# Optimization experiments

Hardware: AMD Instinct MI355X
Metric: run time of the kernel (lower is better)

## Reference

```python
import jax, jax.numpy as jnp
import numpy as np

D_MODEL = 1024
HEADS = 16
D_K = D_MODEL // HEADS
B, S = 2, 2048


def setup_inputs() -> dict:
    key = jax.random.key(0)
    ks = jax.random.split(key, 11)
    sc = 1.0 / np.sqrt(D_MODEL)
    inp = {
        "q": jax.random.normal(ks[0], (B, S, D_MODEL), jnp.float32),
        "k": jax.random.normal(ks[1], (B, S, D_MODEL), jnp.float32),
        "v": jax.random.normal(ks[2], (B, S, D_MODEL), jnp.float32),
        # causal mask, broadcastable to (B, H, S, S); 0 -> masked
        "mask": jnp.tril(jnp.ones((S, S), jnp.int32))[None, None],
        "w_q": jax.random.normal(ks[3], (D_MODEL, D_MODEL), jnp.float32) * sc,
        "b_q": jax.random.normal(ks[4], (D_MODEL,), jnp.float32) * sc,
        "w_k": jax.random.normal(ks[5], (D_MODEL, D_MODEL), jnp.float32) * sc,
        "b_k": jax.random.normal(ks[6], (D_MODEL,), jnp.float32) * sc,
        "w_v": jax.random.normal(ks[7], (D_MODEL, D_MODEL), jnp.float32) * sc,
        "b_v": jax.random.normal(ks[8], (D_MODEL,), jnp.float32) * sc,
        "w_o": jax.random.normal(ks[9], (D_MODEL, D_MODEL), jnp.float32) * sc,
        "b_o": jax.random.normal(ks[10], (D_MODEL,), jnp.float32) * sc,
    }
    return inp


def reference(q, k, v, mask, w_q, b_q, w_k, b_k, w_v, b_v, w_o, b_o):
    b = q.shape[0]
    # torch Linear: x @ W.T + b
    Q = q @ w_q.T + b_q
    K = k @ w_k.T + b_k
    V = v @ w_v.T + b_v
    # (B, S, D) -> (B, H, S, d_k)
    Q = Q.reshape(b, -1, HEADS, D_K).transpose(0, 2, 1, 3)
    K = K.reshape(b, -1, HEADS, D_K).transpose(0, 2, 1, 3)
    V = V.reshape(b, -1, HEADS, D_K).transpose(0, 2, 1, 3)
    scores = jnp.einsum("bhqd,bhkd->bhqk", Q, K) / np.sqrt(D_K).astype(np.float32)
    scores = jnp.where(mask == 0, -jnp.inf, scores)
    attn = jax.nn.softmax(scores, axis=-1)
    out = jnp.einsum("bhqk,bhkd->bhqd", attn, V)
    out = out.transpose(0, 2, 1, 3).reshape(b, -1, D_MODEL)
    # dropout is identity in eval mode
    return out @ w_o.T + b_o
```

## Files before the change

kernel.cpp:

```cpp
#include <hip/hip_runtime.h>
#include <math.h>

#define D_MODEL 1024
#define N_HEADS 16
#define DKH     64
#define BATCH   2
#define SEQ     2048
#define NT      (SEQ/64)

typedef unsigned short u16;
typedef __attribute__((ext_vector_type(8))) short short8;
typedef __attribute__((ext_vector_type(4))) float f32x4;

__device__ __forceinline__ u16 f2bf(float f) {
    unsigned u = __float_as_uint(f);
    u += 0x7fffu + ((u >> 16) & 1u);
    return (u16)(u >> 16);
}

__device__ __forceinline__ void gll16(const void* g, void* l) {
    __builtin_amdgcn_global_load_lds((const __attribute__((address_space(1))) void*)g,
                                     (__attribute__((address_space(3))) void*)l, 16, 0, 0);
}

__global__ __launch_bounds__(256)
void convert_kernel(const float* __restrict__ q, const float* __restrict__ k,
                    const float* __restrict__ v, const float* __restrict__ wq,
                    const float* __restrict__ wk, const float* __restrict__ wv,
                    const float* __restrict__ wo,
                    u16* __restrict__ qb, u16* __restrict__ kb, u16* __restrict__ vb,
                    u16* __restrict__ wqb, u16* __restrict__ wkb,
                    u16* __restrict__ wvb, u16* __restrict__ wob)
{
    const size_t NV = ((size_t)16 << 20) >> 3;
    for (size_t i = (size_t)blockIdx.x * blockDim.x + threadIdx.x; i < NV;
         i += (size_t)gridDim.x * blockDim.x) {
        const size_t e = i << 3;
        const float* s; u16* d; size_t off;
        if (e < ((size_t)12 << 20)) {
            const int seg = (int)(e >> 22);
            off = e & (((size_t)1 << 22) - 1);
            s = seg == 0 ? q : seg == 1 ? k : v;
            d = seg == 0 ? qb : seg == 1 ? kb : vb;
        } else {
            const size_t r = e - ((size_t)12 << 20);
            const int seg = (int)(r >> 20);
            off = r & (((size_t)1 << 20) - 1);
            s = seg == 0 ? wq : seg == 1 ? wk : seg == 2 ? wv : wo;
            d = seg == 0 ? wqb : seg == 1 ? wkb : seg == 2 ? wvb : wob;
        }
        const float4 f0 = *(const float4*)(s + off);
        const float4 f1 = *(const float4*)(s + off + 4);
        short8 o;
        o[0]=(short)f2bf(f0.x); o[1]=(short)f2bf(f0.y); o[2]=(short)f2bf(f0.z); o[3]=(short)f2bf(f0.w);
        o[4]=(short)f2bf(f1.x); o[5]=(short)f2bf(f1.y); o[6]=(short)f2bf(f1.z); o[7]=(short)f2bf(f1.w);
        *(short8*)(d + off) = o;
    }
}

#define GEMM_PREAMBLE                                                            \
    __shared__ __align__(16) u16 As[2][128][32];                                 \
    __shared__ __align__(16) u16 Bs[2][128][32];                                 \
    const int tid  = threadIdx.x;                                                \
    const int lane = tid & 63;                                                   \
    const int wid  = tid >> 6;                                                   \
    const int wm   = wid >> 1, wn = wid & 1;                                     \
    const int lr   = lane & 15, lg = lane >> 4;                                  \
    const int mb   = blockIdx.x * 128, nb = blockIdx.y * 128;                    \
    const int g_row = lane >> 2;                                                 \
    const int g_col = (lane & 3) << 3;                                           \
    const u16* Ab = A  + (size_t)mb * K;                                         \
    const u16* Bb = Bw + (size_t)nb * K;                                         \
    f32x4 acc[4][4];                                                             \
    _Pragma("unroll")                                                            \
    for (int i = 0; i < 4; ++i)                                                  \
        _Pragma("unroll")                                                        \
        for (int j = 0; j < 4; ++j) { f32x4 z = {0.f,0.f,0.f,0.f}; acc[i][j] = z; }

#define STAGE(buf, kt)                                                           \
    {                                                                            \
        _Pragma("unroll")                                                        \
        for (int t = 0; t < 2; ++t) {                                            \
            const int r0 = t*64 + wid*16;                                        \
            gll16(&Ab[(size_t)(r0 + g_row)*K + (kt) + g_col], &As[buf][r0][0]);  \
            gll16(&Bb[(size_t)(r0 + g_row)*K + (kt) + g_col], &Bs[buf][r0][0]);  \
        }                                                                        \
    }

#define GEMM_MAINLOOP                                                            \
    STAGE(0, 0)                                                                  \
    __syncthreads();                                                             \
    const int NK = K >> 5;                                                       \
    for (int it = 0; it < NK; ++it) {                                            \
        const int c = it & 1;                                                    \
        if (it + 1 < NK) STAGE(c ^ 1, (it + 1) << 5)                             \
        short8 a[4], b[4];                                                       \
        _Pragma("unroll")                                                        \
        for (int i = 0; i < 4; ++i) a[i] = *(const short8*)&As[c][wm*64 + i*16 + lr][lg*8]; \
        _Pragma("unroll")                                                        \
        for (int j = 0; j < 4; ++j) b[j] = *(const short8*)&Bs[c][wn*64 + j*16 + lr][lg*8]; \
        _Pragma("unroll")                                                        \
        for (int i = 0; i < 4; ++i)                                              \
            _Pragma("unroll")                                                    \
            for (int j = 0; j < 4; ++j)                                          \
                acc[i][j] = __builtin_amdgcn_mfma_f32_16x16x32_bf16(a[i], b[j], acc[i][j], 0, 0, 0); \
        __syncthreads();                                                         \
    }

__global__ __launch_bounds__(256, 3)
void gemm_qkv_kernel(const u16* __restrict__ qb, const u16* __restrict__ kb,
                     const u16* __restrict__ vb, const u16* __restrict__ wqb,
                     const u16* __restrict__ wkb, const u16* __restrict__ wvb,
                     const float* __restrict__ b_q, const float* __restrict__ b_k,
                     const float* __restrict__ b_v,
                     u16* __restrict__ Qh, u16* __restrict__ Kh, u16* __restrict__ Vt,
                     int M, int N, int K)
{
    const int z = blockIdx.z;
    const u16* A    = z == 0 ? qb  : z == 1 ? kb  : vb;
    const u16* Bw   = z == 0 ? wqb : z == 1 ? wkb : wvb;
    const float* bias = z == 0 ? b_q : z == 1 ? b_k : b_v;
    u16* dst        = z == 0 ? Qh  : z == 1 ? Kh  : Vt;
    const float scale = z == 0 ? 0.125f : 1.0f;

    GEMM_PREAMBLE
    GEMM_MAINLOOP

    #pragma unroll
    for (int i = 0; i < 4; ++i) {
        #pragma unroll
        for (int j = 0; j < 4; ++j) {
            const int mbase = mb + wm*64 + i*16 + lg*4;
            const int n     = nb + wn*64 + j*16 + lr;
            const float bn  = bias[n];
            const int h = n >> 6, d = n & 63;
            #pragma unroll
            for (int r = 0; r < 4; ++r) {
                const int m = mbase + r;
                const int b = m >> 11, s = m & (SEQ - 1);
                const float val = (acc[i][j][r] + bn) * scale;
                if (z == 2)
                    dst[(((size_t)(b*N_HEADS + h))*DKH + d)*SEQ + s] = f2bf(val);
                else
                    dst[(((size_t)(b*N_HEADS + h))*SEQ + s)*DKH + d] = f2bf(val);
            }
        }
    }
}

__global__ __launch_bounds__(256)
void gemm_out_kernel(const u16* __restrict__ A, const u16* __restrict__ Bw,
                     const float* __restrict__ bias, float* __restrict__ dst,
                     int M, int N, int K)
{
    GEMM_PREAMBLE
    GEMM_MAINLOOP

    #pragma unroll
    for (int i = 0; i < 4; ++i) {
        #pragma unroll
        for (int j = 0; j < 4; ++j) {
            const int mbase = mb + wm*64 + i*16 + lg*4;
            const int n     = nb + wn*64 + j*16 + lr;
            const float bn  = bias[n];
            #pragma unroll
            for (int r = 0; r < 4; ++r)
                dst[(size_t)(mbase + r) * N + n] = acc[i][j][r] + bn;
        }
    }
}

__device__ __forceinline__ void attn_step(
    const short8& aq0, const short8& aq1,
    f32x4 (&o)[4], f32x4& osum, float (&m_run)[4],
    const u16 (*__restrict__ Kl)[64], const u16 (*__restrict__ Vl)[64],
    u16 (*__restrict__ Pw)[72],
    int kvb, int qbw, int lr, int lg)
{
    const int ksw = (lr & 7) << 3;
    f32x4 s[4];
    #pragma unroll
    for (int cb = 0; cb < 4; ++cb) {
        const int kr = cb*16 + lr;
        f32x4 z = {0.f,0.f,0.f,0.f};
        short8 k0 = *(const short8*)&Kl[kr][( 0 + lg*8) ^ ksw];
        short8 k1 = *(const short8*)&Kl[kr][(32 + lg*8) ^ ksw];
        z = __builtin_amdgcn_mfma_f32_16x16x32_bf16(aq0, k0, z, 0, 0, 0);
        z = __builtin_amdgcn_mfma_f32_16x16x32_bf16(aq1, k1, z, 0, 0, 0);
        s[cb] = z;
    }

    if (kvb + 63 > qbw) {
        #pragma unroll
        for (int cb = 0; cb < 4; ++cb)
            #pragma unroll
            for (int r = 0; r < 4; ++r)
                if (kvb + cb*16 + lr > qbw + lg*4 + r) s[cb][r] = -INFINITY;
    }

    float tm[4];
    #pragma unroll
    for (int r = 0; r < 4; ++r) {
        float t = fmaxf(fmaxf(s[0][r], s[1][r]), fmaxf(s[2][r], s[3][r]));
        #pragma unroll
        for (int off = 1; off < 16; off <<= 1) t = fmaxf(t, __shfl_xor(t, off));
        tm[r] = t;
    }
    int need = 0;
    #pragma unroll
    for (int r = 0; r < 4; ++r) need |= (tm[r] > m_run[r] + 8.f) ? 1 : 0;
    if (__any(need)) {
        #pragma unroll
        for (int r = 0; r < 4; ++r) {
            const float mnew  = fmaxf(m_run[r], tm[r]);
            const float alpha = __expf(m_run[r] - mnew);
            m_run[r] = mnew;
            osum[r] *= alpha;
            #pragma unroll
            for (int db = 0; db < 4; ++db) o[db][r] *= alpha;
        }
    }
    #pragma unroll
    for (int r = 0; r < 4; ++r)
        #pragma unroll
        for (int cb = 0; cb < 4; ++cb)
            Pw[lg*4 + r][cb*16 + lr] = f2bf(__expf(s[cb][r] - m_run[r]));

    short8 vone;
    #pragma unroll
    for (int j = 0; j < 8; ++j) vone[j] = (short)0x3F80;
    #pragma unroll
    for (int ks = 0; ks < 2; ++ks) {
        short8 ap = *(short8*)&Pw[lr][ks*32 + lg*8];
        #pragma unroll
        for (int db = 0; db < 4; ++db) {
            const int vr = db*16 + lr;
            short8 bv = *(const short8*)&Vl[vr][(ks*32 + lg*8) ^ ksw];
            o[db] = __builtin_amdgcn_mfma_f32_16x16x32_bf16(ap, bv, o[db], 0, 0, 0);
        }
        osum = __builtin_amdgcn_mfma_f32_16x16x32_bf16(ap, vone, osum, 0, 0, 0);
    }
}

__global__ __launch_bounds__(256)
void flash_attn_kernel(const u16* __restrict__ Qh, const u16* __restrict__ Kh,
                       const u16* __restrict__ Vt, u16* __restrict__ attb)
{
    __shared__ __align__(16) u16 Kl[2][64][64];
    __shared__ __align__(16) u16 Vl[2][64][64];
    __shared__ __align__(16) u16 P[4][16][72];

    const int tid  = threadIdx.x;
    const int lane = tid & 63;
    const int wid  = tid >> 6;
    const int lr   = lane & 15, lg = lane >> 4;
    const int qtl  = blockIdx.x;
    const int bh   = blockIdx.y;
    const int qlo  = qtl, qhi = NT - 1 - qtl;
    const int qbw_lo = qlo*64 + wid*16;
    const int qbw_hi = qhi*64 + wid*16;
    const size_t base = (size_t)bh * SEQ * DKH;

    const int srow = tid >> 3;
    const int se0  = (tid & 7) << 3;
    const int sec  = se0 ^ ((srow & 7) << 3);

    short8 aqlo0 = *(const short8*)&Qh[base + (size_t)(qbw_lo + lr)*DKH +  0 + lg*8];
    short8 aqlo1 = *(const short8*)&Qh[base + (size_t)(qbw_lo + lr)*DKH + 32 + lg*8];
    short8 aqhi0 = *(const short8*)&Qh[base + (size_t)(qbw_hi + lr)*DKH +  0 + lg*8];
    short8 aqhi1 = *(const short8*)&Qh[base + (size_t)(qbw_hi + lr)*DKH + 32 + lg*8];

    f32x4 o_lo[4], o_hi[4], osum_lo, osum_hi;
    float m_lo[4], m_hi[4];
    #pragma unroll
    for (int r = 0; r < 4; ++r) { m_lo[r] = -INFINITY; m_hi[r] = -INFINITY; }
    {
        f32x4 z = {0.f,0.f,0.f,0.f};
        osum_lo = z; osum_hi = z;
        #pragma unroll
        for (int db = 0; db < 4; ++db) { o_lo[db] = z; o_hi[db] = z; }
    }

    const int nc = qhi + 1;

    {
        short8 k0 = *(const short8*)&Kh[base + (size_t)(srow     )*DKH + se0];
        short8 k1 = *(const short8*)&Kh[base + (size_t)(srow + 32)*DKH + se0];
        short8 v0 = *(const short8*)&Vt[base + (size_t)(srow     )*SEQ + se0];
        short8 v1 = *(const short8*)&Vt[base + (size_t)(srow + 32)*SEQ + se0];
        *(short8*)&Kl[0][srow     ][sec] = k0;
        *(short8*)&Kl[0][srow + 32][sec] = k1;
        *(short8*)&Vl[0][srow     ][sec] = v0;
        *(short8*)&Vl[0][srow + 32][sec] = v1;
    }
    __syncthreads();

    int cur = 0;
    for (int c = 0; c < nc; ++c) {
        const int kvb = c * 64;
        short8 nk0, nk1, nv0, nv1;
        const bool pref = (c + 1 < nc);
        if (pref) {
            const int nb_ = kvb + 64;
            nk0 = *(const short8*)&Kh[base + (size_t)(nb_ + srow     )*DKH + se0];
            nk1 = *(const short8*)&Kh[base + (size_t)(nb_ + srow + 32)*DKH + se0];
            nv0 = *(const short8*)&Vt[base + (size_t)(srow     )*SEQ + nb_ + se0];
            nv1 = *(const short8*)&Vt[base + (size_t)(srow + 32)*SEQ + nb_ + se0];
        }

        attn_step(aqhi0, aqhi1, o_hi, osum_hi, m_hi, Kl[cur], Vl[cur], P[wid], kvb, qbw_hi, lr, lg);
        if (c <= qlo)
            attn_step(aqlo0, aqlo1, o_lo, osum_lo, m_lo, Kl[cur], Vl[cur], P[wid], kvb, qbw_lo, lr, lg);

        __syncthreads();
        if (pref) {
            *(short8*)&Kl[cur^1][srow     ][sec] = nk0;
            *(short8*)&Kl[cur^1][srow + 32][sec] = nk1;
            *(short8*)&Vl[cur^1][srow     ][sec] = nv0;
            *(short8*)&Vl[cur^1][srow + 32][sec] = nv1;
        }
        __syncthreads();
        cur ^= 1;
    }

    const int b = bh >> 4, h = bh & 15;
    float inv_lo[4], inv_hi[4];
    #pragma unroll
    for (int r = 0; r < 4; ++r) { inv_lo[r] = 1.f / osum_lo[r]; inv_hi[r] = 1.f / osum_hi[r]; }
    #pragma unroll
    for (int db = 0; db < 4; ++db) {
        #pragma unroll
        for (int r = 0; r < 4; ++r) {
            const int slo = qbw_lo + lg*4 + r;
            const int shi = qbw_hi + lg*4 + r;
            attb[((size_t)(b*SEQ + slo))*D_MODEL + h*64 + db*16 + lr] = f2bf(o_lo[db][r] * inv_lo[r]);
            attb[((size_t)(b*SEQ + shi))*D_MODEL + h*64 + db*16 + lr] = f2bf(o_hi[db][r] * inv_hi[r]);
        }
    }
}

extern "C" void kernel_launch(void* const* d_in, const int* in_sizes, int n_in,
                              void* d_out, int out_size, void* d_ws, size_t ws_size,
                              hipStream_t stream)
{
    const float* q   = (const float*)d_in[0];
    const float* k   = (const float*)d_in[1];
    const float* v   = (const float*)d_in[2];
    const float* w_q = (const float*)d_in[4];
    const float* b_q = (const float*)d_in[5];
    const float* w_k = (const float*)d_in[6];
    const float* b_k = (const float*)d_in[7];
    const float* w_v = (const float*)d_in[8];
    const float* b_v = (const float*)d_in[9];
    const float* w_o = (const float*)d_in[10];
    const float* b_o = (const float*)d_in[11];

    char* ws = (char*)d_ws;
    const size_t MB = 1024*1024;
    u16* Qh   = (u16*)(ws +  0*MB);
    u16* Kh   = (u16*)(ws +  8*MB);
    u16* Vt   = (u16*)(ws + 16*MB);
    u16* qb   = (u16*)(ws + 24*MB);
    u16* kb   = (u16*)(ws + 32*MB);
    u16* vb   = (u16*)(ws + 40*MB);
    u16* wqb  = (u16*)(ws + 48*MB);
    u16* wkb  = (u16*)(ws + 50*MB);
    u16* wvb  = (u16*)(ws + 52*MB);
    u16* wob  = (u16*)(ws + 54*MB);
    u16* attb = qb;

    const int M = BATCH * SEQ, N = D_MODEL, K = D_MODEL;

    convert_kernel<<<2048, 256, 0, stream>>>(q, k, v, w_q, w_k, w_v, w_o,
                                             qb, kb, vb, wqb, wkb, wvb, wob);
    gemm_qkv_kernel<<<dim3(M/128, N/128, 3), 256, 0, stream>>>(
        qb, kb, vb, wqb, wkb, wvb, b_q, b_k, b_v, Qh, Kh, Vt, M, N, K);
    flash_attn_kernel<<<dim3(NT/2, BATCH*N_HEADS), 256, 0, stream>>>(Qh, Kh, Vt, attb);
    gemm_out_kernel<<<dim3(M/128, N/128), 256, 0, stream>>>(attb, wob, b_o, (float*)d_out, M, N, K);
}
```

Measured before the change: 145.8 us.

## Restructure flash attention into 128-row query tiles with 8 waves per block

The flash attention kernel no longer pairs a low and a high query tile per block for causal load balance. Each block now has 512 threads (8 waves) covering a contiguous 128-row query tile, with the grid ordered so the heaviest tiles launch first. Each K/V tile staged in LDS is shared by twice as many query rows, and per-thread register state is halved, which allows higher occupancy. In exchange, blocks now do unequal amounts of work, waves sit idle on causally masked chunks but still hit the barriers, and every block pays per-chunk synchronization across 8 waves.

```diff
diff --git a/kernel.cpp b/kernel.cpp
--- a/kernel.cpp
+++ b/kernel.cpp
@@ -242,99 +242,84 @@
     }
 }
 
-__global__ __launch_bounds__(256)
+__global__ __launch_bounds__(512, 4)
 void flash_attn_kernel(const u16* __restrict__ Qh, const u16* __restrict__ Kh,
                        const u16* __restrict__ Vt, u16* __restrict__ attb)
 {
     __shared__ __align__(16) u16 Kl[2][64][64];
     __shared__ __align__(16) u16 Vl[2][64][64];
-    __shared__ __align__(16) u16 P[4][16][72];
+    __shared__ __align__(16) u16 P[8][16][72];
 
     const int tid  = threadIdx.x;
     const int lane = tid & 63;
     const int wid  = tid >> 6;
     const int lr   = lane & 15, lg = lane >> 4;
-    const int qtl  = blockIdx.x;
-    const int bh   = blockIdx.y;
-    const int qlo  = qtl, qhi = NT - 1 - qtl;
-    const int qbw_lo = qlo*64 + wid*16;
-    const int qbw_hi = qhi*64 + wid*16;
+    const int bh   = blockIdx.x;
+    const int t    = 15 - blockIdx.y;
+    const int qbw  = t*128 + wid*16;
     const size_t base = (size_t)bh * SEQ * DKH;
 
     const int srow = tid >> 3;
     const int se0  = (tid & 7) << 3;
     const int sec  = se0 ^ ((srow & 7) << 3);
 
-    short8 aqlo0 = *(const short8*)&Qh[base + (size_t)(qbw_lo + lr)*DKH +  0 + lg*8];
-    short8 aqlo1 = *(const short8*)&Qh[base + (size_t)(qbw_lo + lr)*DKH + 32 + lg*8];
-    short8 aqhi0 = *(const short8*)&Qh[base + (size_t)(qbw_hi + lr)*DKH +  0 + lg*8];
-    short8 aqhi1 = *(const short8*)&Qh[base + (size_t)(qbw_hi + lr)*DKH + 32 + lg*8];
-
-    f32x4 o_lo[4], o_hi[4], osum_lo, osum_hi;
-    float m_lo[4], m_hi[4];
-    #pragma unroll
-    for (int r = 0; r < 4; ++r) { m_lo[r] = -INFINITY; m_hi[r] = -INFINITY; }
+    short8 aq0 = *(const short8*)&Qh[base + (size_t)(qbw + lr)*DKH +  0 + lg*8];
+    short8 aq1 = *(const short8*)&Qh[base + (size_t)(qbw + lr)*DKH + 32 + lg*8];
+
+    f32x4 o[4], osum;
+    float m_run[4];
+    #pragma unroll
+    for (int r = 0; r < 4; ++r) m_run[r] = -INFINITY;
     {
         f32x4 z = {0.f,0.f,0.f,0.f};
-        osum_lo = z; osum_hi = z;
-        #pragma unroll
-        for (int db = 0; db < 4; ++db) { o_lo[db] = z; o_hi[db] = z; }
-    }
-
-    const int nc = qhi + 1;
+        osum = z;
+        #pragma unroll
+        for (int db = 0; db < 4; ++db) o[db] = z;
+    }
+
+    const int nc = 2 * (t + 1);
 
     {
-        short8 k0 = *(const short8*)&Kh[base + (size_t)(srow     )*DKH + se0];
-        short8 k1 = *(const short8*)&Kh[base + (size_t)(srow + 32)*DKH + se0];
-        short8 v0 = *(const short8*)&Vt[base + (size_t)(srow     )*SEQ + se0];
-        short8 v1 = *(const short8*)&Vt[base + (size_t)(srow + 32)*SEQ + se0];
-        *(short8*)&Kl[0][srow     ][sec] = k0;
-        *(short8*)&Kl[0][srow + 32][sec] = k1;
-        *(short8*)&Vl[0][srow     ][sec] = v0;
-        *(short8*)&Vl[0][srow + 32][sec] = v1;
+        short8 k0 = *(const short8*)&Kh[base + (size_t)srow*DKH + se0];
+        short8 v0 = *(const short8*)&Vt[base + (size_t)srow*SEQ + se0];
+        *(short8*)&Kl[0][srow][sec] = k0;
+        *(short8*)&Vl[0][srow][sec] = v0;
     }
     __syncthreads();
 
     int cur = 0;
     for (int c = 0; c < nc; ++c) {
         const int kvb = c * 64;
-        short8 nk0, nk1, nv0, nv1;
+        short8 nk0, nv0;
         const bool pref = (c + 1 < nc);
         if (pref) {
             const int nb_ = kvb + 64;
-            nk0 = *(const short8*)&Kh[base + (size_t)(nb_ + srow     )*DKH + se0];
-            nk1 = *(const short8*)&Kh[base + (size_t)(nb_ + srow + 32)*DKH + se0];
-            nv0 = *(const short8*)&Vt[base + (size_t)(srow     )*SEQ + nb_ + se0];
-            nv1 = *(const short8*)&Vt[base + (size_t)(srow + 32)*SEQ + nb_ + se0];
-        }
-
-        attn_step(aqhi0, aqhi1, o_hi, osum_hi, m_hi, Kl[cur], Vl[cur], P[wid], kvb, qbw_hi, lr, lg);
-        if (c <= qlo)
-            attn_step(aqlo0, aqlo1, o_lo, osum_lo, m_lo, Kl[cur], Vl[cur], P[wid], kvb, qbw_lo, lr, lg);
+            nk0 = *(const short8*)&Kh[base + (size_t)(nb_ + srow)*DKH + se0];
+            nv0 = *(const short8*)&Vt[base + (size_t)srow*SEQ + nb_ + se0];
+        }
+
+        if (kvb <= qbw + 15)
+            attn_step(aq0, aq1, o, osum, m_run, Kl[cur], Vl[cur], P[wid], kvb, qbw, lr, lg);
 
         __syncthreads();
         if (pref) {
-            *(short8*)&Kl[cur^1][srow     ][sec] = nk0;
-            *(short8*)&Kl[cur^1][srow + 32][sec] = nk1;
-            *(short8*)&Vl[cur^1][srow     ][sec] = nv0;
-            *(short8*)&Vl[cur^1][srow + 32][sec] = nv1;
+            *(short8*)&Kl[cur^1][srow][sec] = nk0;
+            *(short8*)&Vl[cur^1][srow][sec] = nv0;
         }
         __syncthreads();
         cur ^= 1;
     }
 
     const int b = bh >> 4, h = bh & 15;
-    float inv_lo[4], inv_hi[4];
-    #pragma unroll
-    for (int r = 0; r < 4; ++r) { inv_lo[r] = 1.f / osum_lo[r]; inv_hi[r] = 1.f / osum_hi[r]; }
+    float inv[4];
+    #pragma unroll
+    for (int r = 0; r < 4; ++r) inv[r] = 1.f / osum[r];
     #pragma unroll
     for (int db = 0; db < 4; ++db) {
         #pragma unroll
         for (int r = 0; r < 4; ++r) {
-            const int slo = qbw_lo + lg*4 + r;
-            const int shi = qbw_hi + lg*4 + r;
-            attb[((size_t)(b*SEQ + slo))*D_MODEL + h*64 + db*16 + lr] = f2bf(o_lo[db][r] * inv_lo[r]);
-            attb[((size_t)(b*SEQ + shi))*D_MODEL + h*64 + db*16 + lr] = f2bf(o_hi[db][r] * inv_hi[r]);
+            const int s_ = qbw + lg*4 + r;
+            attb[((size_t)(b*SEQ + s_))*D_MODEL + h*64 + db*16 + lr] = f2bf(o[db][r] * inv[r]);
         }
     }
 }
@@ -375,6 +360,6 @@
                                              qb, kb, vb, wqb, wkb, wvb, wob);
     gemm_qkv_kernel<<<dim3(M/128, N/128, 3), 256, 0, stream>>>(
         qb, kb, vb, wqb, wkb, wvb, b_q, b_k, b_v, Qh, Kh, Vt, M, N, K);
-    flash_attn_kernel<<<dim3(NT/2, BATCH*N_HEADS), 256, 0, stream>>>(Qh, Kh, Vt, attb);
+    flash_attn_kernel<<<dim3(BATCH*N_HEADS, 16), 512, 0, stream>>>(Qh, Kh, Vt, attb);
     gemm_out_kernel<<<dim3(M/128, N/128), 256, 0, stream>>>(attb, wob, b_o, (float*)d_out, M, N, K);
 }
```

After: 141.2 us. -3.2%, faster.
